# Performance work log

Hardware: AMD Instinct MI355X
Metric: run time of the kernel (lower is better)

The kernel has to match this reference:

```python
import jax, jax.numpy as jnp
import numpy as np

B, S, D = 2, 2048, 1024
H = 16
DH = D // H  # 64


def setup_inputs() -> dict:
    key = jax.random.key(0)
    k1, k2, k3, k4, k5 = jax.random.split(key, 5)
    scale = 1.0 / np.sqrt(D)
    return {
        "x": jax.random.normal(k1, (B, S, D), dtype=jnp.float32),
        "w_in": jax.random.normal(k2, (3 * D, D), dtype=jnp.float32) * scale,
        "b_in": jax.random.normal(k3, (3 * D,), dtype=jnp.float32) * 0.02,
        "w_out": jax.random.normal(k4, (D, D), dtype=jnp.float32) * scale,
        "b_out": jax.random.normal(k5, (D,), dtype=jnp.float32) * 0.02,
        "mask": 1,
    }


def reference(x, w_in, b_in, w_out, b_out, mask):
    bs, seq_len, d_emb = x.shape
    # in_proj: torch Linear -> x @ W^T + b
    qkv = jnp.einsum("bsd,ed->bse", x, w_in) + b_in  # (B, S, 3D)
    q, k, v = jnp.split(qkv, 3, axis=-1)
    # (B, S, D) -> (B, H, S, DH)
    def heads(t):
        return t.reshape(bs, seq_len, H, DH).transpose(0, 2, 1, 3)
    q, k, v = heads(q), heads(k), heads(v)
    scores = jnp.einsum("bhqd,bhkd->bhqk", q, k)  # (B, H, S, S)
    if mask:
        causal = jnp.triu(jnp.ones((seq_len, seq_len), dtype=bool), k=1)
        scores = jnp.where(causal, -jnp.inf, scores)
    # original divides after masking; -inf / scale is still -inf
    scores = scores / jnp.sqrt(jnp.asarray(DH, dtype=scores.dtype))
    weights = jax.nn.softmax(scores, axis=-1)
    att = jnp.einsum("bhqk,bhkd->bhqd", weights, v)  # (B, H, S, DH)
    att = att.transpose(0, 2, 1, 3).reshape(bs, seq_len, d_emb)
    out = jnp.einsum("bsd,ed->bse", att, w_out) + b_out
    return out
```

## Files before the change

kernel.cpp:

```cpp
#include <hip/hip_runtime.h>
#include <hip/hip_bf16.h>
#include <stdint.h>


typedef __attribute__((ext_vector_type(8))) short bf16x8;
typedef __attribute__((ext_vector_type(4))) float f32x4;
typedef __attribute__((ext_vector_type(16))) float f32x16;
typedef __attribute__((ext_vector_type(4))) unsigned int u32x4;

typedef const __attribute__((address_space(1))) uint32_t* gp1_t;
typedef __attribute__((address_space(3))) uint32_t* lp3_t;

static __device__ __forceinline__ uint32_t cvtpk(float lo, float hi) {
  uint32_t r;
  asm("v_cvt_pk_bf16_f32 %0, %1, %2" : "=v"(r) : "v"(lo), "v"(hi));
  return r;
}
static __device__ __forceinline__ uint16_t f2b(float x) {
  return (uint16_t)cvtpk(x, x);
}
static __device__ __forceinline__ float fexp2(float x) {
  float r;
  asm("v_exp_f32 %0, %1" : "=v"(r) : "v"(x));
  return r;
}

template <int ISSUES>
static __device__ __forceinline__ void stage64(const uint16_t* __restrict__ g, int gstride,
                                               uint8_t* lds, int t) {
#pragma unroll
  for (int i = 0; i < ISSUES; ++i) {
    int p = i * 256 + t;
    int row = p >> 3, c = p & 7;
    const uint16_t* src = g + row * gstride + ((c ^ (row & 7)) << 3);
    __builtin_amdgcn_global_load_lds((gp1_t)src, (lp3_t)(lds + (p & ~63) * 16), 16, 0, 0);
  }
}

static __device__ __forceinline__ bf16x8 ld_frag(const uint8_t* lds, int row, int chunk) {
  return *(const bf16x8*)(lds + row * 128 + (((chunk) ^ (row & 7)) << 4));
}

__global__ __launch_bounds__(256) void cvt3(const float* __restrict__ a,
                                            const float* __restrict__ b,
                                            const float* __restrict__ c,
                                            uint16_t* __restrict__ oa,
                                            uint16_t* __restrict__ ob,
                                            uint16_t* __restrict__ oc) {
  int i = blockIdx.x * 256 + threadIdx.x;
  const float* src;
  uint16_t* dst;
  int j;
  if (i < 1048576)      { src = a; dst = oa; j = i; }
  else if (i < 1835008) { src = b; dst = ob; j = i - 1048576; }
  else                  { src = c; dst = oc; j = i - 1835008; }
  float4 v = ((const float4*)src)[j];
  uint2 o;
  o.x = cvtpk(v.x, v.y);
  o.y = cvtpk(v.z, v.w);
  ((uint2*)dst)[j] = o;
}

__global__ __launch_bounds__(256) void gemm_qkv(const uint16_t* __restrict__ A,
                                                const uint16_t* __restrict__ W,
                                                const float* __restrict__ bias,
                                                uint16_t* __restrict__ Qb,
                                                uint16_t* __restrict__ Kb,
                                                uint16_t* __restrict__ Vt) {
  __shared__ uint8_t smraw[49152];
  int t = threadIdx.x, l = t & 63, w = t >> 6;
  int bid = (int)blockIdx.x + 48 * (int)blockIdx.y;
  int virt = (bid & 7) * 192 + (bid >> 3);
  int bx = virt % 48, by = virt / 48;
  int m0 = by * 128, n0 = bx * 64;
  int wr = (w >> 1) * 64, wc = (w & 1) * 32;
  const f32x4 fz = {0.f, 0.f, 0.f, 0.f};
  f32x4 acc[4][2];
#pragma unroll
  for (int i = 0; i < 4; ++i)
#pragma unroll
    for (int j = 0; j < 2; ++j) acc[i][j] = fz;

  const uint16_t* Ab_ = A + m0 * 1024;
  const uint16_t* Wb_ = W + n0 * 1024;
  stage64<4>(Ab_, 1024, smraw, t);
  stage64<2>(Wb_, 1024, smraw + 16384, t);

  for (int kt = 0; kt < 16; ++kt) {
    int cur = kt & 1;
    uint8_t* curb = smraw + cur * 24576;
    asm volatile("s_waitcnt vmcnt(0)" ::: "memory");
    __syncthreads();
    if (kt + 1 < 16) {
      uint8_t* nb = smraw + (cur ^ 1) * 24576;
      stage64<4>(Ab_ + (kt + 1) * 64, 1024, nb, t);
      stage64<2>(Wb_ + (kt + 1) * 64, 1024, nb + 16384, t);
    }
#pragma unroll
    for (int ks = 0; ks < 2; ++ks) {
      bf16x8 a[4], b[2];
#pragma unroll
      for (int i = 0; i < 4; ++i)
        a[i] = ld_frag(curb, wr + i * 16 + (l & 15), ks * 4 + (l >> 4));
#pragma unroll
      for (int j = 0; j < 2; ++j)
        b[j] = ld_frag(curb + 16384, wc + j * 16 + (l & 15), ks * 4 + (l >> 4));
#pragma unroll
      for (int i = 0; i < 4; ++i)
#pragma unroll
        for (int j = 0; j < 2; ++j)
          acc[i][j] = __builtin_amdgcn_mfma_f32_16x16x32_bf16(a[i], b[j], acc[i][j], 0, 0, 0);
    }
  }

  __syncthreads();
  uint16_t* ot = (uint16_t*)smraw;
  const float CSQ = 0.18033688011112042f;
  int sec = n0 >> 10;
#pragma unroll
  for (int j = 0; j < 2; ++j) {
    int col = wc + j * 16 + (l & 15);
    float bv = bias[n0 + col];
#pragma unroll
    for (int i = 0; i < 4; ++i) {
      int rb = wr + i * 16 + ((l >> 4) << 2);
#pragma unroll
      for (int r = 0; r < 4; ++r) {
        int row = rb + r;
        float v = acc[i][j][r] + bv;
        if (sec == 0) v *= CSQ;
        if (sec == 2) {
          int rowp = (row & ~12) | ((row & 4) << 1) | ((row & 8) >> 1);
          ot[col * 136 + rowp] = f2b(v);
        } else {
          ot[row * 72 + col] = f2b(v);
        }
      }
    }
  }
  __syncthreads();

  int bb0 = m0 >> 11, sbase = m0 & 2047;
  int h = (n0 & 1023) >> 6;
  if (sec < 2) {
    uint16_t* dst0 = (sec == 0) ? Qb : Kb;
    int s_loc = t >> 1, half = t & 1;
    const uint16_t* src = ot + s_loc * 72 + half * 32;
    uint16_t* dst = dst0 + (((size_t)((bb0 * 16 + h) * 2048 + sbase + s_loc)) << 6) + half * 32;
#pragma unroll
    for (int c = 0; c < 4; ++c)
      *(u32x4*)(dst + c * 8) = *(const u32x4*)(src + c * 8);
  } else {
    int dh = t >> 2, qr = t & 3;
    const uint16_t* src = ot + dh * 136 + qr * 32;
    uint16_t* dst = Vt + ((size_t)((bb0 * 16 + h) * 64 + dh)) * 2048 + sbase + qr * 32;
#pragma unroll
    for (int c = 0; c < 4; ++c)
      *(u32x4*)(dst + c * 8) = *(const u32x4*)(src + c * 8);
  }
}

__global__ __launch_bounds__(256) void gemm_out(const uint16_t* __restrict__ A,
                                                const uint16_t* __restrict__ W,
                                                const float* __restrict__ bias,
                                                float* __restrict__ out) {
  __shared__ uint8_t sm[49152];
  int t = threadIdx.x, l = t & 63, w = t >> 6;
  int bid = (int)blockIdx.x + 16 * (int)blockIdx.y;
  int virt = (bid & 7) * 64 + (bid >> 3);
  int bx = virt % 16, by = virt / 16;
  int m0 = by * 128, n0 = bx * 64;
  int wr = (w >> 1) * 64, wc = (w & 1) * 32;
  const f32x4 fz = {0.f, 0.f, 0.f, 0.f};
  f32x4 acc[4][2];
#pragma unroll
  for (int i = 0; i < 4; ++i)
#pragma unroll
    for (int j = 0; j < 2; ++j) acc[i][j] = fz;

  const uint16_t* Ab_ = A + m0 * 1024;
  const uint16_t* Wb_ = W + n0 * 1024;
  stage64<4>(Ab_, 1024, sm, t);
  stage64<2>(Wb_, 1024, sm + 16384, t);

  for (int kt = 0; kt < 16; ++kt) {
    int cur = kt & 1;
    uint8_t* curb = sm + cur * 24576;
    asm volatile("s_waitcnt vmcnt(0)" ::: "memory");
    __syncthreads();
    if (kt + 1 < 16) {
      uint8_t* nb = sm + (cur ^ 1) * 24576;
      stage64<4>(Ab_ + (kt + 1) * 64, 1024, nb, t);
      stage64<2>(Wb_ + (kt + 1) * 64, 1024, nb + 16384, t);
    }
#pragma unroll
    for (int ks = 0; ks < 2; ++ks) {
      bf16x8 a[4], b[2];
#pragma unroll
      for (int i = 0; i < 4; ++i)
        a[i] = ld_frag(curb, wr + i * 16 + (l & 15), ks * 4 + (l >> 4));
#pragma unroll
      for (int j = 0; j < 2; ++j)
        b[j] = ld_frag(curb + 16384, wc + j * 16 + (l & 15), ks * 4 + (l >> 4));
#pragma unroll
      for (int i = 0; i < 4; ++i)
#pragma unroll
        for (int j = 0; j < 2; ++j)
          acc[i][j] = __builtin_amdgcn_mfma_f32_16x16x32_bf16(a[i], b[j], acc[i][j], 0, 0, 0);
    }
  }
#pragma unroll
  for (int j = 0; j < 2; ++j) {
    int e = n0 + wc + j * 16 + (l & 15);
    float bv = bias[e];
#pragma unroll
    for (int i = 0; i < 4; ++i) {
      int mb = m0 + wr + i * 16 + ((l >> 4) << 2);
#pragma unroll
      for (int r = 0; r < 4; ++r) {
        int m = mb + r;
        out[m * 1024 + e] = acc[i][j][r] + bv;
      }
    }
  }
}

__global__ __launch_bounds__(512) void attn(const uint16_t* __restrict__ Qb,
                                            const uint16_t* __restrict__ Kb,
                                            const uint16_t* __restrict__ Vt,
                                            uint16_t* __restrict__ Ab,
                                            const int* __restrict__ maskp) {
  __shared__ uint8_t smem[65536];
  int t = threadIdx.x, l = t & 63, w = t >> 6;
  int hi = l >> 5, ql = l & 31;
  int g = w >> 2, wg = w & 3;
  int tl = t & 255;
  int did = (int)blockIdx.x;
  int xcd = did & 7, idx = did >> 3;
  int st = 15 - (idx >> 2);
  int bh = xcd * 4 + (idx & 3);
  bool causal = (*maskp != 0);
  int rounds = causal ? (st + 1) : 16;
  int tile0 = g * rounds;
  int q0w = st * 128 + wg * 32;
  int q = q0w + ql;
  int bb = bh >> 4, h = bh & 15;

  const uint16_t* KpB = Kb + ((size_t)bh << 17);
  const uint16_t* VpB = Vt + ((size_t)bh << 17);
  uint8_t* gbuf = smem + (g << 15);

  bf16x8 qf[4];
  const uint16_t* Qp = Qb + (((size_t)bh * 2048 + q) << 6) + hi * 8;
#pragma unroll
  for (int ks = 0; ks < 4; ++ks) qf[ks] = *(const bf16x8*)(Qp + ks * 16);

  f32x16 acco[2];
#pragma unroll
  for (int r = 0; r < 16; ++r) { acco[0][r] = 0.f; acco[1][r] = 0.f; }
  float lsum = 0.f;

  stage64<2>(KpB + ((size_t)tile0 << 12), 64, gbuf, tl);
  stage64<2>(VpB + tile0 * 64, 2048, gbuf + 8192, tl);

  for (int rr = 0; rr < rounds; ++rr) {
    int tt = tile0 + rr;
    int cur = rr & 1;
    asm volatile("s_waitcnt vmcnt(0)" ::: "memory");
    __syncthreads();
    if (rr + 1 < rounds) {
      uint8_t* nb = gbuf + ((cur ^ 1) << 14);
      stage64<2>(KpB + ((size_t)(tt + 1) << 12), 64, nb, tl);
      stage64<2>(VpB + (tt + 1) * 64, 2048, nb + 8192, tl);
    }
    if (causal && tt * 64 > q0w + 31) continue;

    const uint8_t* Ks = gbuf + (cur << 14);
    const uint8_t* Vs = Ks + 8192;
    bf16x8 kf[2][4], vf[2][4];
#pragma unroll
    for (int ks = 0; ks < 4; ++ks) {
      kf[0][ks] = ld_frag(Ks, ql,      ks * 2 + hi);
      kf[1][ks] = ld_frag(Ks, 32 + ql, ks * 2 + hi);
      vf[0][ks] = ld_frag(Vs, ql,      ks * 2 + hi);
      vf[1][ks] = ld_frag(Vs, 32 + ql, ks * 2 + hi);
    }

    f32x16 sc[2];
#pragma unroll
    for (int r = 0; r < 16; ++r) { sc[0][r] = 0.f; sc[1][r] = 0.f; }
    __builtin_amdgcn_s_setprio(1);
#pragma unroll
    for (int ks = 0; ks < 4; ++ks)
      sc[0] = __builtin_amdgcn_mfma_f32_32x32x16_bf16(kf[0][ks], qf[ks], sc[0], 0, 0, 0);
#pragma unroll
    for (int ks = 0; ks < 4; ++ks)
      sc[1] = __builtin_amdgcn_mfma_f32_32x32x16_bf16(kf[1][ks], qf[ks], sc[1], 0, 0, 0);
    __builtin_amdgcn_s_setprio(0);

    bool nomask = (!causal) || (tt * 64 + 63 <= q0w);
    int qrel = q - tt * 64;
    float rs0 = 0.f, rs1 = 0.f, rs2 = 0.f, rs3 = 0.f;

#pragma unroll
    for (int r = 0; r < 16; ++r) {
      float v = sc[0][r];
      if (!nomask) {
        int kv = (r & 3) + 8 * (r >> 2) + 4 * hi;
        v = (kv <= qrel) ? v : -1e30f;
      }
      float e = fexp2(v);
      sc[0][r] = e;
      if (r & 1) rs1 += e; else rs0 += e;
    }

    __builtin_amdgcn_s_setprio(1);
#pragma unroll
    for (int ks = 0; ks < 2; ++ks) {
      int a8 = ks * 8;
      u32x4 wv = {cvtpk(sc[0][a8 + 0], sc[0][a8 + 1]),
                  cvtpk(sc[0][a8 + 2], sc[0][a8 + 3]),
                  cvtpk(sc[0][a8 + 4], sc[0][a8 + 5]),
                  cvtpk(sc[0][a8 + 6], sc[0][a8 + 7])};
      bf16x8 af = __builtin_bit_cast(bf16x8, wv);
      acco[0] = __builtin_amdgcn_mfma_f32_32x32x16_bf16(af, vf[0][ks], acco[0], 0, 0, 0);
      acco[1] = __builtin_amdgcn_mfma_f32_32x32x16_bf16(af, vf[1][ks], acco[1], 0, 0, 0);
    }
    __builtin_amdgcn_s_setprio(0);

#pragma unroll
    for (int r = 0; r < 16; ++r) {
      float v = sc[1][r];
      if (!nomask) {
        int kv = 32 + (r & 3) + 8 * (r >> 2) + 4 * hi;
        v = (kv <= qrel) ? v : -1e30f;
      }
      float e = fexp2(v);
      sc[1][r] = e;
      if (r & 1) rs3 += e; else rs2 += e;
    }

    __builtin_amdgcn_s_setprio(1);
#pragma unroll
    for (int ks = 0; ks < 2; ++ks) {
      int a8 = ks * 8;
      u32x4 wv = {cvtpk(sc[1][a8 + 0], sc[1][a8 + 1]),
                  cvtpk(sc[1][a8 + 2], sc[1][a8 + 3]),
                  cvtpk(sc[1][a8 + 4], sc[1][a8 + 5]),
                  cvtpk(sc[1][a8 + 6], sc[1][a8 + 7])};
      bf16x8 af = __builtin_bit_cast(bf16x8, wv);
      acco[0] = __builtin_amdgcn_mfma_f32_32x32x16_bf16(af, vf[0][ks + 2], acco[0], 0, 0, 0);
      acco[1] = __builtin_amdgcn_mfma_f32_32x32x16_bf16(af, vf[1][ks + 2], acco[1], 0, 0, 0);
    }
    __builtin_amdgcn_s_setprio(0);

    lsum += (rs0 + rs1) + (rs2 + rs3);
  }

  __syncthreads();
  lsum += __shfl_xor(lsum, 32);
  float (*oaccS)[64][33] = (float(*)[64][33])smem;
  float (*lsumS)[64]     = (float(*)[64])(smem + 33792);
  if (g == 1) {
#pragma unroll
    for (int r = 0; r < 16; ++r) {
      oaccS[wg][l][r] = acco[0][r];
      oaccS[wg][l][16 + r] = acco[1][r];
    }
    lsumS[wg][l] = lsum;
  }
  __syncthreads();
  if (g == 0) {
#pragma unroll
    for (int r = 0; r < 16; ++r) {
      acco[0][r] += oaccS[wg][l][r];
      acco[1][r] += oaccS[wg][l][16 + r];
    }
    lsum += lsumS[wg][l];
#pragma unroll
    for (int r = 0; r < 16; ++r) {
      int crow = (r & 3) + 8 * (r >> 2) + 4 * hi;
      float L = __shfl(lsum, crow);
      float inv = 1.0f / L;
      int qg = q0w + crow;
#pragma unroll
      for (int n = 0; n < 2; ++n)
        Ab[(((size_t)(bb * 2048 + qg)) << 10) + h * 64 + n * 32 + ql] = f2b(acco[n][r] * inv);
    }
  }
}

extern "C" void kernel_launch(void* const* d_in, const int* in_sizes, int n_in,
                              void* d_out, int out_size, void* d_ws, size_t ws_size,
                              hipStream_t stream) {
  const float* x     = (const float*)d_in[0];
  const float* w_in  = (const float*)d_in[1];
  const float* b_in  = (const float*)d_in[2];
  const float* w_out = (const float*)d_in[3];
  const float* b_out = (const float*)d_in[4];
  const int*   mask  = (const int*)d_in[5];
  float* out = (float*)d_out;

  uint8_t* ws = (uint8_t*)d_ws;
  uint16_t* xb  = (uint16_t*)(ws);
  uint16_t* wib = (uint16_t*)(ws + (8u << 20));
  uint16_t* wob = (uint16_t*)(ws + (14u << 20));
  uint16_t* Qb  = (uint16_t*)(ws + (16u << 20));
  uint16_t* Kb  = (uint16_t*)(ws + (24u << 20));
  uint16_t* Vt  = (uint16_t*)(ws + (32u << 20));
  uint16_t* Ab  = (uint16_t*)(ws + (40u << 20));

  cvt3<<<8192, 256, 0, stream>>>(x, w_in, w_out, xb, wib, wob);
  gemm_qkv<<<dim3(48, 32), 256, 0, stream>>>(xb, wib, b_in, Qb, Kb, Vt);
  attn<<<512, 512, 0, stream>>>(Qb, Kb, Vt, Ab, mask);
  gemm_out<<<dim3(16, 32), 256, 0, stream>>>(Ab, wob, b_out, out);
}
```

Measured before the change: 112.1 us.

## Give each attention wave 64 query rows to reuse K/V fragments

The attention block shrinks from 8 waves to 4, and each wave now handles two 32-row query blocks instead of one. Every K and V fragment read from LDS feeds two MFMAs, which halves LDS fragment traffic per unit of compute. The cost is more accumulator registers per wave and fewer waves to hide latency. Causal skipping also becomes coarser at 64-row granularity, so some masked work is no longer skipped.

```diff
diff --git a/kernel.cpp b/kernel.cpp
--- a/kernel.cpp
+++ b/kernel.cpp
@@ -25,12 +25,12 @@
   return r;
 }
 
-template <int ISSUES>
+template <int ISSUES, int THR = 256>
 static __device__ __forceinline__ void stage64(const uint16_t* __restrict__ g, int gstride,
                                                uint8_t* lds, int t) {
 #pragma unroll
   for (int i = 0; i < ISSUES; ++i) {
-    int p = i * 256 + t;
+    int p = i * THR + t;
     int row = p >> 3, c = p & 7;
     const uint16_t* src = g + row * gstride + ((c ^ (row & 7)) << 3);
     __builtin_amdgcn_global_load_lds((gp1_t)src, (lp3_t)(lds + (p & ~63) * 16), 16, 0, 0);
@@ -225,7 +225,7 @@
   }
 }
 
-__global__ __launch_bounds__(512) void attn(const uint16_t* __restrict__ Qb,
+__global__ __launch_bounds__(256) void attn(const uint16_t* __restrict__ Qb,
                                             const uint16_t* __restrict__ Kb,
                                             const uint16_t* __restrict__ Vt,
                                             uint16_t* __restrict__ Ab,
@@ -233,8 +233,8 @@
   __shared__ uint8_t smem[65536];
   int t = threadIdx.x, l = t & 63, w = t >> 6;
   int hi = l >> 5, ql = l & 31;
-  int g = w >> 2, wg = w & 3;
-  int tl = t & 255;
+  int g = w >> 1, wg = w & 1;
+  int tl = t & 127;
   int did = (int)blockIdx.x;
   int xcd = did & 7, idx = did >> 3;
   int st = 15 - (idx >> 2);
@@ -242,26 +242,32 @@
   bool causal = (*maskp != 0);
   int rounds = causal ? (st + 1) : 16;
   int tile0 = g * rounds;
-  int q0w = st * 128 + wg * 32;
-  int q = q0w + ql;
+  int q0w = st * 128 + wg * 64;
   int bb = bh >> 4, h = bh & 15;
 
   const uint16_t* KpB = Kb + ((size_t)bh << 17);
   const uint16_t* VpB = Vt + ((size_t)bh << 17);
   uint8_t* gbuf = smem + (g << 15);
 
-  bf16x8 qf[4];
-  const uint16_t* Qp = Qb + (((size_t)bh * 2048 + q) << 6) + hi * 8;
-#pragma unroll
-  for (int ks = 0; ks < 4; ++ks) qf[ks] = *(const bf16x8*)(Qp + ks * 16);
-
-  f32x16 acco[2];
-#pragma unroll
-  for (int r = 0; r < 16; ++r) { acco[0][r] = 0.f; acco[1][r] = 0.f; }
-  float lsum = 0.f;
-
-  stage64<2>(KpB + ((size_t)tile0 << 12), 64, gbuf, tl);
-  stage64<2>(VpB + tile0 * 64, 2048, gbuf + 8192, tl);
+  bf16x8 qf[2][4];
+#pragma unroll
+  for (int qb = 0; qb < 2; ++qb) {
+    const uint16_t* Qp = Qb + (((size_t)(bh * 2048 + q0w + qb * 32 + ql)) << 6) + hi * 8;
+#pragma unroll
+    for (int ks = 0; ks < 4; ++ks) qf[qb][ks] = *(const bf16x8*)(Qp + ks * 16);
+  }
+
+  f32x16 acc[2][2];
+#pragma unroll
+  for (int qb = 0; qb < 2; ++qb)
+#pragma unroll
+    for (int n = 0; n < 2; ++n)
+#pragma unroll
+      for (int r = 0; r < 16; ++r) acc[qb][n][r] = 0.f;
+  float lsum0 = 0.f, lsum1 = 0.f;
+
+  stage64<4, 128>(KpB + ((size_t)tile0 << 12), 64, gbuf, tl);
+  stage64<4, 128>(VpB + tile0 * 64, 2048, gbuf + 8192, tl);
 
   for (int rr = 0; rr < rounds; ++rr) {
     int tt = tile0 + rr;
@@ -270,122 +276,111 @@
     __syncthreads();
     if (rr + 1 < rounds) {
       uint8_t* nb = gbuf + ((cur ^ 1) << 14);
-      stage64<2>(KpB + ((size_t)(tt + 1) << 12), 64, nb, tl);
-      stage64<2>(VpB + (tt + 1) * 64, 2048, nb + 8192, tl);
-    }
-    if (causal && tt * 64 > q0w + 31) continue;
+      stage64<4, 128>(KpB + ((size_t)(tt + 1) << 12), 64, nb, tl);
+      stage64<4, 128>(VpB + (tt + 1) * 64, 2048, nb + 8192, tl);
+    }
+    if (causal && tt * 64 > q0w + 63) continue;
 
     const uint8_t* Ks = gbuf + (cur << 14);
     const uint8_t* Vs = Ks + 8192;
-    bf16x8 kf[2][4], vf[2][4];
-#pragma unroll
-    for (int ks = 0; ks < 4; ++ks) {
-      kf[0][ks] = ld_frag(Ks, ql,      ks * 2 + hi);
-      kf[1][ks] = ld_frag(Ks, 32 + ql, ks * 2 + hi);
-      vf[0][ks] = ld_frag(Vs, ql,      ks * 2 + hi);
-      vf[1][ks] = ld_frag(Vs, 32 + ql, ks * 2 + hi);
-    }
-
-    f32x16 sc[2];
-#pragma unroll
-    for (int r = 0; r < 16; ++r) { sc[0][r] = 0.f; sc[1][r] = 0.f; }
-    __builtin_amdgcn_s_setprio(1);
-#pragma unroll
-    for (int ks = 0; ks < 4; ++ks)
-      sc[0] = __builtin_amdgcn_mfma_f32_32x32x16_bf16(kf[0][ks], qf[ks], sc[0], 0, 0, 0);
-#pragma unroll
-    for (int ks = 0; ks < 4; ++ks)
-      sc[1] = __builtin_amdgcn_mfma_f32_32x32x16_bf16(kf[1][ks], qf[ks], sc[1], 0, 0, 0);
-    __builtin_amdgcn_s_setprio(0);
-
-    bool nomask = (!causal) || (tt * 64 + 63 <= q0w);
-    int qrel = q - tt * 64;
-    float rs0 = 0.f, rs1 = 0.f, rs2 = 0.f, rs3 = 0.f;
-
-#pragma unroll
-    for (int r = 0; r < 16; ++r) {
-      float v = sc[0][r];
-      if (!nomask) {
-        int kv = (r & 3) + 8 * (r >> 2) + 4 * hi;
-        v = (kv <= qrel) ? v : -1e30f;
-      }
-      float e = fexp2(v);
-      sc[0][r] = e;
-      if (r & 1) rs1 += e; else rs0 += e;
-    }
-
-    __builtin_amdgcn_s_setprio(1);
-#pragma unroll
-    for (int ks = 0; ks < 2; ++ks) {
-      int a8 = ks * 8;
-      u32x4 wv = {cvtpk(sc[0][a8 + 0], sc[0][a8 + 1]),
-                  cvtpk(sc[0][a8 + 2], sc[0][a8 + 3]),
-                  cvtpk(sc[0][a8 + 4], sc[0][a8 + 5]),
-                  cvtpk(sc[0][a8 + 6], sc[0][a8 + 7])};
-      bf16x8 af = __builtin_bit_cast(bf16x8, wv);
-      acco[0] = __builtin_amdgcn_mfma_f32_32x32x16_bf16(af, vf[0][ks], acco[0], 0, 0, 0);
-      acco[1] = __builtin_amdgcn_mfma_f32_32x32x16_bf16(af, vf[1][ks], acco[1], 0, 0, 0);
-    }
-    __builtin_amdgcn_s_setprio(0);
-
-#pragma unroll
-    for (int r = 0; r < 16; ++r) {
-      float v = sc[1][r];
-      if (!nomask) {
-        int kv = 32 + (r & 3) + 8 * (r >> 2) + 4 * hi;
-        v = (kv <= qrel) ? v : -1e30f;
-      }
-      float e = fexp2(v);
-      sc[1][r] = e;
-      if (r & 1) rs3 += e; else rs2 += e;
-    }
-
-    __builtin_amdgcn_s_setprio(1);
-#pragma unroll
-    for (int ks = 0; ks < 2; ++ks) {
-      int a8 = ks * 8;
-      u32x4 wv = {cvtpk(sc[1][a8 + 0], sc[1][a8 + 1]),
-                  cvtpk(sc[1][a8 + 2], sc[1][a8 + 3]),
-                  cvtpk(sc[1][a8 + 4], sc[1][a8 + 5]),
-                  cvtpk(sc[1][a8 + 6], sc[1][a8 + 7])};
-      bf16x8 af = __builtin_bit_cast(bf16x8, wv);
-      acco[0] = __builtin_amdgcn_mfma_f32_32x32x16_bf16(af, vf[0][ks + 2], acco[0], 0, 0, 0);
-      acco[1] = __builtin_amdgcn_mfma_f32_32x32x16_bf16(af, vf[1][ks + 2], acco[1], 0, 0, 0);
-    }
-    __builtin_amdgcn_s_setprio(0);
-
-    lsum += (rs0 + rs1) + (rs2 + rs3);
+    int qrel0 = q0w + ql - tt * 64;
+
+#pragma unroll
+    for (int f = 0; f < 2; ++f) {
+      f32x16 sc0, sc1;
+#pragma unroll
+      for (int r = 0; r < 16; ++r) { sc0[r] = 0.f; sc1[r] = 0.f; }
+      __builtin_amdgcn_s_setprio(1);
+#pragma unroll
+      for (int ks = 0; ks < 4; ++ks) {
+        bf16x8 kfr = ld_frag(Ks, f * 32 + ql, ks * 2 + hi);
+        sc0 = __builtin_amdgcn_mfma_f32_32x32x16_bf16(kfr, qf[0][ks], sc0, 0, 0, 0);
+        sc1 = __builtin_amdgcn_mfma_f32_32x32x16_bf16(kfr, qf[1][ks], sc1, 0, 0, 0);
+      }
+      __builtin_amdgcn_s_setprio(0);
+
+      bool nm0 = (!causal) || (tt * 64 + f * 32 + 31 <= q0w);
+      bool nm1 = (!causal) || (tt * 64 + f * 32 + 31 <= q0w + 32);
+      float rsa = 0.f, rsb = 0.f;
+#pragma unroll
+      for (int r = 0; r < 16; ++r) {
+        int kvr = f * 32 + (r & 3) + 8 * (r >> 2) + 4 * hi;
+        float v0 = sc0[r];
+        if (!nm0) v0 = (kvr <= qrel0) ? v0 : -1e30f;
+        float e0 = fexp2(v0);
+        sc0[r] = e0;
+        rsa += e0;
+        float v1 = sc1[r];
+        if (!nm1) v1 = (kvr <= qrel0 + 32) ? v1 : -1e30f;
+        float e1 = fexp2(v1);
+        sc1[r] = e1;
+        rsb += e1;
+      }
+      lsum0 += rsa;
+      lsum1 += rsb;
+
+      __builtin_amdgcn_s_setprio(1);
+#pragma unroll
+      for (int k2 = 0; k2 < 2; ++k2) {
+        int a8 = k2 * 8;
+        u32x4 w0 = {cvtpk(sc0[a8 + 0], sc0[a8 + 1]), cvtpk(sc0[a8 + 2], sc0[a8 + 3]),
+                    cvtpk(sc0[a8 + 4], sc0[a8 + 5]), cvtpk(sc0[a8 + 6], sc0[a8 + 7])};
+        u32x4 w1 = {cvtpk(sc1[a8 + 0], sc1[a8 + 1]), cvtpk(sc1[a8 + 2], sc1[a8 + 3]),
+                    cvtpk(sc1[a8 + 4], sc1[a8 + 5]), cvtpk(sc1[a8 + 6], sc1[a8 + 7])};
+        bf16x8 a0 = __builtin_bit_cast(bf16x8, w0);
+        bf16x8 a1 = __builtin_bit_cast(bf16x8, w1);
+#pragma unroll
+        for (int n = 0; n < 2; ++n) {
+          bf16x8 vfr = ld_frag(Vs, n * 32 + ql, (f * 2 + k2) * 2 + hi);
+          acc[0][n] = __builtin_amdgcn_mfma_f32_32x32x16_bf16(a0, vfr, acc[0][n], 0, 0, 0);
+          acc[1][n] = __builtin_amdgcn_mfma_f32_32x32x16_bf16(a1, vfr, acc[1][n], 0, 0, 0);
+        }
+      }
+      __builtin_amdgcn_s_setprio(0);
+    }
   }
 
   __syncthreads();
-  lsum += __shfl_xor(lsum, 32);
-  float (*oaccS)[64][33] = (float(*)[64][33])smem;
-  float (*lsumS)[64]     = (float(*)[64])(smem + 33792);
+  lsum0 += __shfl_xor(lsum0, 32);
+  lsum1 += __shfl_xor(lsum1, 32);
+  float (*oaccS)[64][65] = (float(*)[64][65])smem;
+  float (*lsumS)[64][2]  = (float(*)[64][2])(smem + 34816);
   if (g == 1) {
 #pragma unroll
-    for (int r = 0; r < 16; ++r) {
-      oaccS[wg][l][r] = acco[0][r];
-      oaccS[wg][l][16 + r] = acco[1][r];
-    }
-    lsumS[wg][l] = lsum;
+    for (int qb = 0; qb < 2; ++qb)
+#pragma unroll
+      for (int n = 0; n < 2; ++n)
+#pragma unroll
+        for (int r = 0; r < 16; ++r)
+          oaccS[wg][l][qb * 32 + n * 16 + r] = acc[qb][n][r];
+    lsumS[wg][l][0] = lsum0;
+    lsumS[wg][l][1] = lsum1;
   }
   __syncthreads();
   if (g == 0) {
 #pragma unroll
-    for (int r = 0; r < 16; ++r) {
-      acco[0][r] += oaccS[wg][l][r];
-      acco[1][r] += oaccS[wg][l][16 + r];
-    }
-    lsum += lsumS[wg][l];
-#pragma unroll
-    for (int r = 0; r < 16; ++r) {
-      int crow = (r & 3) + 8 * (r >> 2) + 4 * hi;
-      float L = __shfl(lsum, crow);
-      float inv = 1.0f / L;
-      int qg = q0w + crow;
+    for (int qb = 0; qb < 2; ++qb)
 #pragma unroll
       for (int n = 0; n < 2; ++n)
-        Ab[(((size_t)(bb * 2048 + qg)) << 10) + h * 64 + n * 32 + ql] = f2b(acco[n][r] * inv);
+#pragma unroll
+        for (int r = 0; r < 16; ++r)
+          acc[qb][n][r] += oaccS[wg][l][qb * 32 + n * 16 + r];
+    lsum0 += lsumS[wg][l][0];
+    lsum1 += lsumS[wg][l][1];
+#pragma unroll
+    for (int qb = 0; qb < 2; ++qb) {
+      float ls = qb ? lsum1 : lsum0;
+#pragma unroll
+      for (int r = 0; r < 16; ++r) {
+        int crow = (r & 3) + 8 * (r >> 2) + 4 * hi;
+        float L = __shfl(ls, crow);
+        float inv = 1.0f / L;
+        int qg = q0w + qb * 32 + crow;
+#pragma unroll
+        for (int n = 0; n < 2; ++n)
+          Ab[(((size_t)(bb * 2048 + qg)) << 10) + h * 64 + n * 32 + ql] =
+              f2b(acc[qb][n][r] * inv);
+      }
     }
   }
 }
@@ -412,6 +407,6 @@
 
   cvt3<<<8192, 256, 0, stream>>>(x, w_in, w_out, xb, wib, wob);
   gemm_qkv<<<dim3(48, 32), 256, 0, stream>>>(xb, wib, b_in, Qb, Kb, Vt);
-  attn<<<512, 512, 0, stream>>>(Qb, Kb, Vt, Ab, mask);
+  attn<<<512, 256, 0, stream>>>(Qb, Kb, Vt, Ab, mask);
   gemm_out<<<dim3(16, 32), 256, 0, stream>>>(Ab, wob, b_out, out);
 }
```

Result: slower. 121.4 us (+8.3%).
